# Optimization experiments

Hardware: AMD Instinct MI355X
Metric: run time of the kernel (lower is better)

The kernel has to match this reference:

```python
import jax, jax.numpy as jnp
import numpy as np

B, NS, NN = 1024, 1, 64
F = 128            # feat_dim = edge_dim = time_dim = pos_dim
DM = 4 * F         # model_dim = 512
H, DK = 2, 256     # n_head, d_k = d_v = model_dim // n_head
LN_EPS = 1e-5


def setup_inputs() -> dict:
    key = jax.random.key(0)
    ks = jax.random.split(key, 20)
    s = 0.02
    inp = {
        'src':   jax.random.normal(ks[0], (B, NS, F), jnp.float32),
        'src_t': jax.random.normal(ks[1], (B, NS, F), jnp.float32),
        'src_p': jax.random.normal(ks[2], (B, NS, F), jnp.float32),
        'seq':   jax.random.normal(ks[3], (B, NN, F), jnp.float32),
        'seq_t': jax.random.normal(ks[4], (B, NN, F), jnp.float32),
        'seq_e': jax.random.normal(ks[5], (B, NN, F), jnp.float32),
        'seq_p': jax.random.normal(ks[6], (B, NN, F), jnp.float32),
        'mask':  jax.random.randint(ks[7], (B, NS, NN), 0, 2).astype(bool),
        # MapBasedMultiHeadAttention params
        'wq': jax.random.normal(ks[8], (H * DK, DM), jnp.float32) * s,
        'wk': jax.random.normal(ks[9], (H * DK, DM), jnp.float32) * s,
        'wv': jax.random.normal(ks[10], (H * DK, DM), jnp.float32) * s,
        'wm': jax.random.normal(ks[11], (2 * DK,), jnp.float32) * s,   # weight_map: Linear(2*d_k, 1, bias=False)
        'fc_w': jax.random.normal(ks[12], (DM, H * DK), jnp.float32) * s,
        'fc_b': jnp.zeros((DM,), jnp.float32),
        'ln_g': jnp.ones((DM,), jnp.float32),
        'ln_b': jnp.zeros((DM,), jnp.float32),
        # MergeLayer(model_dim, feat_dim, feat_dim, feat_dim)
        'm1_w': jax.random.normal(ks[13], (F, DM + F), jnp.float32) * s,
        'm1_b': jnp.zeros((F,), jnp.float32),
        'm2_w': jax.random.normal(ks[14], (F, F), jnp.float32) * s,
        'm2_b': jnp.zeros((F,), jnp.float32),
    }
    return inp


def reference(src, src_t, src_p, seq, seq_t, seq_e, seq_p, mask,
              wq, wk, wv, wm, fc_w, fc_b, ln_g, ln_b, m1_w, m1_b, m2_w, m2_b):
    b, ns, f = src.shape
    nn = seq.shape[1]
    src_e = jnp.zeros((b, ns, f), src.dtype)  # edge feats of sources are zero
    q = jnp.concatenate([src, src_e, src_t, src_p], axis=-1)   # [B,NS,DM]
    k = jnp.concatenate([seq, seq_e, seq_t, seq_p], axis=-1)   # [B,NN,DM]

    # per-head projections: weight [H*DK, DM] -> [H, DK, DM]
    qh = jnp.einsum('bsd,hed->bshe', q, wq.reshape(H, DK, DM))  # [B,NS,H,DK]
    kh = jnp.einsum('bnd,hed->bnhe', k, wk.reshape(H, DK, DM))  # [B,NN,H,DK]
    vh = jnp.einsum('bnd,hed->bnhe', k, wv.reshape(H, DK, DM))  # [B,NN,H,DK]

    # weight_map(Linear over concat([q,k])) == q @ wm[:DK] + k @ wm[DK:]
    score_q = jnp.einsum('bshe,e->bhs', qh, wm[:DK])            # [B,H,NS]
    score_k = jnp.einsum('bnhe,e->bhn', kh, wm[DK:])            # [B,H,NN]
    attn = score_q[..., None] + score_k[:, :, None, :]          # [B,H,NS,NN]
    attn = jnp.where(mask[:, None, :, :], jnp.float32(-1e10), attn)
    attn = jax.nn.softmax(attn, axis=-1)

    out = jnp.einsum('bhsn,bnhe->bshe', attn, vh).reshape(b, ns, H * DK)
    out = jnp.einsum('bsd,ed->bse', out, fc_w) + fc_b           # fc
    out = jnp.where(out >= 0, out, 0.2 * out)                   # LeakyReLU(0.2)
    out = out + q                                               # residual
    mu = out.mean(axis=-1, keepdims=True)
    var = out.var(axis=-1, keepdims=True)
    out = (out - mu) / jnp.sqrt(var + LN_EPS) * ln_g + ln_b     # LayerNorm

    # MergeLayer (non_linear=True)
    x = jnp.concatenate([out, src], axis=-1)                    # [B,NS,DM+F]
    hdn = jax.nn.relu(jnp.einsum('bsd,ed->bse', x, m1_w) + m1_b)
    z = jnp.einsum('bsd,ed->bse', hdn, m2_w) + m2_b             # [B,NS,F]

    # attn in original layout: [n_head*B, len_q, len_k]
    attn_flat = attn.transpose(1, 0, 2, 3).reshape(H * b, ns, nn)
    return (z, attn_flat)
```

## Files before the change

kernel.cpp:

```cpp
#include <hip/hip_runtime.h>
#include <hip/hip_bf16.h>
#include <stdint.h>

#define B_   1024
#define NN_  64
#define F_   128
#define DM_  512
#define DK_  256

typedef unsigned short u16;
using f32x4  = __attribute__((ext_vector_type(4))) float;
using bf16x8 = __attribute__((ext_vector_type(8))) short;

__device__ __forceinline__ uint32_t f2bf(float x) {
  uint32_t u = __builtin_bit_cast(uint32_t, x);
  return (u + 0x7fffu + ((u >> 16) & 1u)) >> 16;
}
__device__ __forceinline__ float bf2f(uint32_t us) {
  return __builtin_bit_cast(float, us << 16);
}
__device__ __forceinline__ void split_pack(float x, float y, uint32_t& hp, uint32_t& lp) {
  uint32_t hx = f2bf(x), hy = f2bf(y);
  uint32_t lx = f2bf(x - bf2f(hx)), ly = f2bf(y - bf2f(hy));
  hp = hx | (hy << 16);
  lp = lx | (ly << 16);
}
__device__ __forceinline__ void split1(float x, u16& h, u16& l) {
  uint32_t hx = f2bf(x);
  h = (u16)hx;
  l = (u16)f2bf(x - bf2f(hx));
}

__global__ __launch_bounds__(256) void k_prep(
    const float* __restrict__ wv, const float* __restrict__ fc_w,
    const float* __restrict__ m1_w, const float* __restrict__ m2_w,
    const float* __restrict__ wk, const float* __restrict__ wm,
    u16* __restrict__ fc_hi, u16* __restrict__ fc_lo,
    u16* __restrict__ wvT_hi, u16* __restrict__ wvT_lo,
    u16* __restrict__ m1_hi, u16* __restrict__ m1_lo,
    u16* __restrict__ m2_hi, u16* __restrict__ m2_lo,
    float* __restrict__ wkc) {
  __shared__ float tile[32][33];
  int tid = threadIdx.x;
  int bx = blockIdx.x;

  if (bx >= 256) {
    int t = bx - 256;
    int h = t >> 3, dc = t & 7;
    int w = tid >> 6, l = tid & 63;
    int d = dc * 64 + l;
    const float* base = wk + (size_t)(h * DK_ + w * 64) * DM_ + d;
    float sacc[8] = {0.f, 0.f, 0.f, 0.f, 0.f, 0.f, 0.f, 0.f};
    #pragma unroll
    for (int e = 0; e < 64; ++e)
      sacc[e & 7] += base[e * DM_] * wm[DK_ + w * 64 + e];
    float s = ((sacc[0] + sacc[1]) + (sacc[2] + sacc[3])) +
              ((sacc[4] + sacc[5]) + (sacc[6] + sacc[7]));
    float* part = &tile[0][0];
    part[w * 64 + l] = s;
    __syncthreads();
    if (w == 0)
      wkc[h * DM_ + d] = part[l] + part[64 + l] + part[128 + l] + part[192 + l];
    return;
  }

  int gtid = bx * 256 + tid;
  int nthr = 256 * 256;
  for (int i = gtid; i < DM_ * DM_; i += nthr) split1(fc_w[i], fc_hi[i], fc_lo[i]);
  for (int i = gtid; i < F_ * (DM_ + F_); i += nthr) split1(m1_w[i], m1_hi[i], m1_lo[i]);
  for (int i = gtid; i < F_ * F_; i += nthr) split1(m2_w[i], m2_hi[i], m2_lo[i]);

  int e0 = (bx >> 4) * 32, d0 = (bx & 15) * 32;
  int rr = tid >> 3, c4 = (tid & 7) * 4;
  float4 v = *(const float4*)(wv + (e0 + rr) * DM_ + d0 + c4);
  tile[rr][c4] = v.x; tile[rr][c4 + 1] = v.y;
  tile[rr][c4 + 2] = v.z; tile[rr][c4 + 3] = v.w;
  __syncthreads();
  int dr = tid >> 3, ec = (tid & 7) * 4;
  #pragma unroll
  for (int q = 0; q < 4; ++q) {
    int idx = (d0 + dr) * DM_ + e0 + ec + q;
    split1(tile[ec + q][dr], wvT_hi[idx], wvT_lo[idx]);
  }
}

__device__ __forceinline__ f32x4 mfma_tile_split(
    const u16* __restrict__ Ahi, const u16* __restrict__ Alo, int lda,
    const u16* __restrict__ Bhi, const u16* __restrict__ Blo, int ldb, int K) {
  int l = threadIdx.x & 63;
  int r = l & 15, g = l >> 4;
  int offA = r * lda + g * 8;
  int offB = r * ldb + g * 8;
  f32x4 acc = {0.f, 0.f, 0.f, 0.f};
  for (int k = 0; k < K; k += 32) {
    bf16x8 ah = *(const bf16x8*)(Ahi + offA + k);
    bf16x8 al = *(const bf16x8*)(Alo + offA + k);
    bf16x8 bh = *(const bf16x8*)(Bhi + offB + k);
    bf16x8 bl = *(const bf16x8*)(Blo + offB + k);
    acc = __builtin_amdgcn_mfma_f32_16x16x32_bf16(ah, bh, acc, 0, 0, 0);
    acc = __builtin_amdgcn_mfma_f32_16x16x32_bf16(ah, bl, acc, 0, 0, 0);
    acc = __builtin_amdgcn_mfma_f32_16x16x32_bf16(al, bh, acc, 0, 0, 0);
  }
  return acc;
}

__global__ __launch_bounds__(256) void k_wcomb(
    const u16* __restrict__ fc_hi, const u16* __restrict__ fc_lo,
    const u16* __restrict__ wvT_hi, const u16* __restrict__ wvT_lo,
    u16* __restrict__ wc_hi, u16* __restrict__ wc_lo) {
  int wid = threadIdx.x >> 6;
  int n0g = blockIdx.y * 32;
  int h = n0g >> 9, d0 = n0g & 511;
  int m0 = blockIdx.x * 32 + (wid >> 1) * 16;
  int nb = d0 + (wid & 1) * 16;
  f32x4 acc = mfma_tile_split(fc_hi + m0 * DM_ + h * DK_,
                              fc_lo + m0 * DM_ + h * DK_, DM_,
                              wvT_hi + nb * DM_ + h * DK_,
                              wvT_lo + nb * DM_ + h * DK_, DM_, DK_);
  int l = threadIdx.x & 63, r = l & 15, g = l >> 4;
  #pragma unroll
  for (int i = 0; i < 4; ++i) {
    int m = m0 + g * 4 + i;
    int idx = m * 1024 + n0g + (wid & 1) * 16 + r;
    split1(acc[i], wc_hi[idx], wc_lo[idx]);
  }
}

__global__ __launch_bounds__(256) void k_attn(
    const float* __restrict__ seq, const float* __restrict__ seq_e,
    const float* __restrict__ seq_t, const float* __restrict__ seq_p,
    const int* __restrict__ mask, const float* __restrict__ wkc,
    float* __restrict__ attn_out,
    uint32_t* __restrict__ kbar_hi, uint32_t* __restrict__ kbar_lo) {
  __shared__ u16 kls[64][512];
  __shared__ u16 wkb_hi[1024], wkb_lo[1024];
  __shared__ float sb[2][64];
  __shared__ float els[2][64];
  __shared__ float Zs[2];
  __shared__ int mlds[64];
  int tid = threadIdx.x, b = blockIdx.x;
  int ww = tid >> 6, l = tid & 63;
  int r16 = l & 15, kg = l >> 4;

  #pragma unroll
  for (int j = 0; j < 4; ++j) {
    int i = tid * 4 + j;
    split1(wkc[i], wkb_hi[i], wkb_lo[i]);
  }
  if (tid < 64) mlds[tid] = mask[b * 64 + tid];
  __syncthreads();

  int row = ww * 16 + r16;
  int rsw = (row & 7);
  const size_t rb = ((size_t)b * 64 + row) * 128;

  f32x4 acc = {0.f, 0.f, 0.f, 0.f};
  #pragma unroll
  for (int kk4 = 0; kk4 < 4; ++kk4) {
    float4 va[4], vb[4];
    #pragma unroll
    for (int s = 0; s < 4; ++s) {
      int kk = kk4 * 4 + s;
      int d = kk * 32 + kg * 8;
      const float* ap = (d < 128 ? seq : (d < 256 ? seq_e : (d < 384 ? seq_t : seq_p)))
                        + rb + (d & 127);
      va[s] = *(const float4*)ap;
      vb[s] = *(const float4*)(ap + 4);
    }
    #pragma unroll
    for (int s = 0; s < 4; ++s) {
      int kk = kk4 * 4 + s;
      int d = kk * 32 + kg * 8;
      int chunk = d >> 3;
      bf16x8 kh;
      kh[0] = (short)f2bf(va[s].x); kh[1] = (short)f2bf(va[s].y);
      kh[2] = (short)f2bf(va[s].z); kh[3] = (short)f2bf(va[s].w);
      kh[4] = (short)f2bf(vb[s].x); kh[5] = (short)f2bf(vb[s].y);
      kh[6] = (short)f2bf(vb[s].z); kh[7] = (short)f2bf(vb[s].w);
      *(bf16x8*)(&kls[row][(chunk ^ rsw) * 8]) = kh;
      int wo = (r16 & 1) * 512 + d;
      bf16x8 wh = *(const bf16x8*)&wkb_hi[wo];
      bf16x8 wl = *(const bf16x8*)&wkb_lo[wo];
      acc = __builtin_amdgcn_mfma_f32_16x16x32_bf16(kh, wh, acc, 0, 0, 0);
      acc = __builtin_amdgcn_mfma_f32_16x16x32_bf16(kh, wl, acc, 0, 0, 0);
    }
  }
  if (r16 < 2) {
    #pragma unroll
    for (int i = 0; i < 4; ++i)
      sb[r16][ww * 16 + kg * 4 + i] = acc[i];
  }
  __syncthreads();

  if (tid < 128) {
    int h = tid >> 6, rr = tid & 63;
    float s = sb[h][rr];
    float e = mlds[rr] ? 0.f : expf(s);
    els[h][rr] = e;
    float z = e;
    #pragma unroll
    for (int off = 32; off; off >>= 1) z += __shfl_xor(z, off);
    attn_out[(h * B_ + b) * 64 + rr] = e / z;
    if (rr == 0) Zs[h] = z;
  }
  __syncthreads();

  int L = tid;
  int ch = L >> 2, bo = 2 * (L & 3);
  float a00 = 0.f, a01 = 0.f, a10 = 0.f, a11 = 0.f;
  #pragma unroll 8
  for (int j = 0; j < 64; ++j) {
    uint32_t u = *(const uint32_t*)&kls[j][((ch ^ (j & 7))) * 8 + bo];
    float f0 = bf2f(u & 0xffffu), f1 = bf2f(u >> 16);
    float e0 = els[0][j], e1 = els[1][j];
    a00 += e0 * f0; a01 += e0 * f1;
    a10 += e1 * f0; a11 += e1 * f1;
  }
  float r0 = 1.f / Zs[0], r1 = 1.f / Zs[1];
  uint32_t hp, lp;
  int idx = b * 512 + L;
  split_pack(a00 * r0, a01 * r0, hp, lp);
  kbar_hi[idx] = hp; kbar_lo[idx] = lp;
  split_pack(a10 * r1, a11 * r1, hp, lp);
  kbar_hi[idx + 256] = hp; kbar_lo[idx + 256] = lp;
}

__global__ __launch_bounds__(256) void k_fc(
    const u16* __restrict__ kb_hi, const u16* __restrict__ kb_lo,
    const u16* __restrict__ wc_hi, const u16* __restrict__ wc_lo,
    const float* __restrict__ fc_b,
    const float* __restrict__ src, const float* __restrict__ src_t,
    const float* __restrict__ src_p, float* __restrict__ fco) {
  int tid = threadIdx.x;
  int wid = tid >> 6, l = tid & 63;
  int r = l & 15, g = l >> 4;
  int m0 = blockIdx.x * 32 + (wid >> 1) * 16;
  int n0 = blockIdx.y * 64 + (wid & 1) * 32;
  int offA  = (m0 + r) * 1024 + g * 8;
  int offB0 = (n0 + r) * 1024 + g * 8;
  int offB1 = offB0 + 16 * 1024;
  f32x4 acc0 = {0.f, 0.f, 0.f, 0.f}, acc1 = {0.f, 0.f, 0.f, 0.f};
  #pragma unroll 4
  for (int k = 0; k < 1024; k += 32) {
    bf16x8 ah  = *(const bf16x8*)(kb_hi + offA + k);
    bf16x8 al  = *(const bf16x8*)(kb_lo + offA + k);
    bf16x8 b0h = *(const bf16x8*)(wc_hi + offB0 + k);
    bf16x8 b0l = *(const bf16x8*)(wc_lo + offB0 + k);
    bf16x8 b1h = *(const bf16x8*)(wc_hi + offB1 + k);
    bf16x8 b1l = *(const bf16x8*)(wc_lo + offB1 + k);
    acc0 = __builtin_amdgcn_mfma_f32_16x16x32_bf16(ah, b0h, acc0, 0, 0, 0);
    acc0 = __builtin_amdgcn_mfma_f32_16x16x32_bf16(ah, b0l, acc0, 0, 0, 0);
    acc0 = __builtin_amdgcn_mfma_f32_16x16x32_bf16(al, b0h, acc0, 0, 0, 0);
    acc1 = __builtin_amdgcn_mfma_f32_16x16x32_bf16(ah, b1h, acc1, 0, 0, 0);
    acc1 = __builtin_amdgcn_mfma_f32_16x16x32_bf16(ah, b1l, acc1, 0, 0, 0);
    acc1 = __builtin_amdgcn_mfma_f32_16x16x32_bf16(al, b1h, acc1, 0, 0, 0);
  }
  #pragma unroll
  for (int f = 0; f < 2; ++f) {
    int col = n0 + f * 16 + r;
    int part = col >> 7, fc2 = col & 127;
    float bias = fc_b[col];
    const float* qsrc = (part == 0 ? src : (part == 2 ? src_t : src_p));
    #pragma unroll
    for (int i = 0; i < 4; ++i) {
      int m = m0 + g * 4 + i;
      float c = (f == 0 ? acc0[i] : acc1[i]) + bias;
      c = (c >= 0.f) ? c : 0.2f * c;
      float qv = (part == 1) ? 0.f : qsrc[m * 128 + fc2];
      fco[m * 512 + col] = c + qv;
    }
  }
}

__global__ __launch_bounds__(512) void k_m12(
    const float* __restrict__ fco, const float* __restrict__ ln_g,
    const float* __restrict__ ln_b, const float* __restrict__ src,
    const u16* __restrict__ m1_hi, const u16* __restrict__ m1_lo,
    const float* __restrict__ m1_b,
    const u16* __restrict__ m2_hi, const u16* __restrict__ m2_lo,
    const float* __restrict__ m2_b, float* __restrict__ z) {
  __shared__ u16 xh[16][648], xl[16][648];
  __shared__ u16 hh[16][136], hl[16][136];
  int tid = threadIdx.x;
  int m0 = blockIdx.x * 16;

  {
    int row = tid >> 5, l32 = tid & 31;
    int grow = m0 + row;
    float v[16];
    float s = 0.f, s2 = 0.f;
    #pragma unroll
    for (int q = 0; q < 16; ++q) {
      v[q] = fco[grow * 512 + q * 32 + l32];
      s += v[q]; s2 += v[q] * v[q];
    }
    #pragma unroll
    for (int off = 16; off; off >>= 1) {
      s += __shfl_xor(s, off, 32);
      s2 += __shfl_xor(s2, off, 32);
    }
    float mu = s * (1.f / 512.f);
    float var = s2 * (1.f / 512.f) - mu * mu;
    float rstd = rsqrtf(var + 1e-5f);
    #pragma unroll
    for (int q = 0; q < 16; ++q) {
      int col = q * 32 + l32;
      float o = (v[q] - mu) * rstd * ln_g[col] + ln_b[col];
      split1(o, xh[row][col], xl[row][col]);
    }
    #pragma unroll
    for (int q2 = 0; q2 < 4; ++q2) {
      int c = q2 * 32 + l32;
      split1(src[grow * 128 + c], xh[row][512 + c], xl[row][512 + c]);
    }
  }
  __syncthreads();

  int wid = tid >> 6, l = tid & 63;
  int r = l & 15, g = l >> 4;
  int nb = wid * 16;
  {
    f32x4 acc = mfma_tile_split(&xh[0][0], &xl[0][0], 648,
                                m1_hi + nb * 640, m1_lo + nb * 640, 640, 640);
    int col = nb + r;
    float bias = m1_b[col];
    #pragma unroll
    for (int ii = 0; ii < 4; ++ii) {
      int row = g * 4 + ii;
      float o = fmaxf(acc[ii] + bias, 0.f);
      split1(o, hh[row][col], hl[row][col]);
    }
  }
  __syncthreads();
  {
    f32x4 acc = mfma_tile_split(&hh[0][0], &hl[0][0], 136,
                                m2_hi + nb * 128, m2_lo + nb * 128, 128, 128);
    int col = nb + r;
    float bias = m2_b[col];
    #pragma unroll
    for (int ii = 0; ii < 4; ++ii) {
      int row = g * 4 + ii;
      z[(m0 + row) * 128 + col] = acc[ii] + bias;
    }
  }
}

extern "C" void kernel_launch(void* const* d_in, const int* in_sizes, int n_in,
                              void* d_out, int out_size, void* d_ws, size_t ws_size,
                              hipStream_t stream) {
  (void)in_sizes; (void)n_in; (void)out_size; (void)ws_size;
  const float* src   = (const float*)d_in[0];
  const float* src_t = (const float*)d_in[1];
  const float* src_p = (const float*)d_in[2];
  const float* seq   = (const float*)d_in[3];
  const float* seq_t = (const float*)d_in[4];
  const float* seq_e = (const float*)d_in[5];
  const float* seq_p = (const float*)d_in[6];
  const int*   mask  = (const int*)d_in[7];
  const float* wk   = (const float*)d_in[9];
  const float* wv   = (const float*)d_in[10];
  const float* wm   = (const float*)d_in[11];
  const float* fc_w = (const float*)d_in[12];
  const float* fc_b = (const float*)d_in[13];
  const float* ln_g = (const float*)d_in[14];
  const float* ln_b = (const float*)d_in[15];
  const float* m1_w = (const float*)d_in[16];
  const float* m1_b = (const float*)d_in[17];
  const float* m2_w = (const float*)d_in[18];
  const float* m2_b = (const float*)d_in[19];

  float* z_out    = (float*)d_out;
  float* attn_out = z_out + B_ * F_;

  char* ws = (char*)d_ws;
  float* wkc     = (float*)(ws + 0);
  u16* fc_hi     = (u16*)(ws + 4096);
  u16* fc_lo     = (u16*)(ws + 528384);
  u16* m1_hi     = (u16*)(ws + 1052672);
  u16* m1_lo     = (u16*)(ws + 1216512);
  u16* m2_hi     = (u16*)(ws + 1380352);
  u16* m2_lo     = (u16*)(ws + 1413120);
  u16* wvT_hi    = (u16*)(ws + 1445888);
  u16* wvT_lo    = (u16*)(ws + 1970176);
  u16* wc_hi     = (u16*)(ws + 2494464);
  u16* wc_lo     = (u16*)(ws + 3543040);
  uint32_t* kbhi = (uint32_t*)(ws + 4591616);
  uint32_t* kblo = (uint32_t*)(ws + 6688768);
  float* fco     = (float*)(ws + 8785920);

  hipLaunchKernelGGL(k_prep, dim3(272), dim3(256), 0, stream,
                     wv, fc_w, m1_w, m2_w, wk, wm,
                     fc_hi, fc_lo, wvT_hi, wvT_lo,
                     m1_hi, m1_lo, m2_hi, m2_lo, wkc);
  hipLaunchKernelGGL(k_attn, dim3(1024), dim3(256), 0, stream,
                     seq, seq_e, seq_t, seq_p, mask, wkc,
                     attn_out, kbhi, kblo);
  hipLaunchKernelGGL(k_wcomb, dim3(16, 32), dim3(256), 0, stream,
                     fc_hi, fc_lo, wvT_hi, wvT_lo, wc_hi, wc_lo);
  hipLaunchKernelGGL(k_fc, dim3(32, 8), dim3(256), 0, stream,
                     (const u16*)kbhi, (const u16*)kblo, wc_hi, wc_lo, fc_b,
                     src, src_t, src_p, fco);
  hipLaunchKernelGGL(k_m12, dim3(64), dim3(512), 0, stream,
                     fco, ln_g, ln_b, src,
                     m1_hi, m1_lo, m1_b, m2_hi, m2_lo, m2_b, z_out);
}
```

Before: 82.62 us.

## Drop LDS key tile in k_attn; re-read fp32 keys from global for weighted sum

Removes the 64KB bf16 shared-memory copy of the key rows. The attention-weighted key sum now re-reads fp32 keys from global memory (mostly L2 hits), prefetching the next chunk under a software double buffer. Plain __syncthreads is replaced by an LDS-only waitcnt plus s_barrier so outstanding global loads are not drained at the barriers. This lowers LDS use per block, which should allow more resident blocks, and keeps full fp32 precision in the weighted sum. The cost is extra global/L2 traffic and more registers held by the prefetch buffers.

```diff
diff --git a/kernel.cpp b/kernel.cpp
--- a/kernel.cpp
+++ b/kernel.cpp
@@ -29,6 +29,10 @@
   uint32_t hx = f2bf(x);
   h = (u16)hx;
   l = (u16)f2bf(x - bf2f(hx));
+}
+__device__ __forceinline__ void bar_lgkm() {
+  asm volatile("s_waitcnt lgkmcnt(0)" ::: "memory");
+  __builtin_amdgcn_s_barrier();
 }
 
 __global__ __launch_bounds__(256) void k_prep(
@@ -132,7 +136,6 @@
     const int* __restrict__ mask, const float* __restrict__ wkc,
     float* __restrict__ attn_out,
     uint32_t* __restrict__ kbar_hi, uint32_t* __restrict__ kbar_lo) {
-  __shared__ u16 kls[64][512];
   __shared__ u16 wkb_hi[1024], wkb_lo[1024];
   __shared__ float sb[2][64];
   __shared__ float els[2][64];
@@ -150,8 +153,8 @@
   if (tid < 64) mlds[tid] = mask[b * 64 + tid];
   __syncthreads();
 
+  const float* arr = (ww == 0 ? seq : (ww == 1 ? seq_e : (ww == 2 ? seq_t : seq_p)));
   int row = ww * 16 + r16;
-  int rsw = (row & 7);
   const size_t rb = ((size_t)b * 64 + row) * 128;
 
   f32x4 acc = {0.f, 0.f, 0.f, 0.f};
@@ -160,8 +163,7 @@
     float4 va[4], vb[4];
     #pragma unroll
     for (int s = 0; s < 4; ++s) {
-      int kk = kk4 * 4 + s;
-      int d = kk * 32 + kg * 8;
+      int d = (kk4 * 4 + s) * 32 + kg * 8;
       const float* ap = (d < 128 ? seq : (d < 256 ? seq_e : (d < 384 ? seq_t : seq_p)))
                         + rb + (d & 127);
       va[s] = *(const float4*)ap;
@@ -169,15 +171,12 @@
     }
     #pragma unroll
     for (int s = 0; s < 4; ++s) {
-      int kk = kk4 * 4 + s;
-      int d = kk * 32 + kg * 8;
-      int chunk = d >> 3;
+      int d = (kk4 * 4 + s) * 32 + kg * 8;
       bf16x8 kh;
       kh[0] = (short)f2bf(va[s].x); kh[1] = (short)f2bf(va[s].y);
       kh[2] = (short)f2bf(va[s].z); kh[3] = (short)f2bf(va[s].w);
       kh[4] = (short)f2bf(vb[s].x); kh[5] = (short)f2bf(vb[s].y);
       kh[6] = (short)f2bf(vb[s].z); kh[7] = (short)f2bf(vb[s].w);
-      *(bf16x8*)(&kls[row][(chunk ^ rsw) * 8]) = kh;
       int wo = (r16 & 1) * 512 + d;
       bf16x8 wh = *(const bf16x8*)&wkb_hi[wo];
       bf16x8 wl = *(const bf16x8*)&wkb_lo[wo];
@@ -190,7 +189,14 @@
     for (int i = 0; i < 4; ++i)
       sb[r16][ww * 16 + kg * 4 + i] = acc[i];
   }
-  __syncthreads();
+
+  const float* colp = arr + (size_t)b * 8192 + 2 * l;
+  float2 v[8];
+  #pragma unroll
+  for (int u = 0; u < 8; ++u)
+    v[u] = *(const float2*)(colp + (size_t)u * 128);
+
+  bar_lgkm();
 
   if (tid < 128) {
     int h = tid >> 6, rr = tid & 63;
@@ -203,22 +209,31 @@
     attn_out[(h * B_ + b) * 64 + rr] = e / z;
     if (rr == 0) Zs[h] = z;
   }
-  __syncthreads();
-
-  int L = tid;
-  int ch = L >> 2, bo = 2 * (L & 3);
+  bar_lgkm();
+
   float a00 = 0.f, a01 = 0.f, a10 = 0.f, a11 = 0.f;
-  #pragma unroll 8
-  for (int j = 0; j < 64; ++j) {
-    uint32_t u = *(const uint32_t*)&kls[j][((ch ^ (j & 7))) * 8 + bo];
-    float f0 = bf2f(u & 0xffffu), f1 = bf2f(u >> 16);
-    float e0 = els[0][j], e1 = els[1][j];
-    a00 += e0 * f0; a01 += e0 * f1;
-    a10 += e1 * f0; a11 += e1 * f1;
+  for (int jb = 0; jb < 64; jb += 8) {
+    float2 vn[8];
+    if (jb < 56) {
+      #pragma unroll
+      for (int u = 0; u < 8; ++u)
+        vn[u] = *(const float2*)(colp + (size_t)(jb + 8 + u) * 128);
+    }
+    #pragma unroll
+    for (int u = 0; u < 8; ++u) {
+      int j = jb + u;
+      float e0 = els[0][j], e1 = els[1][j];
+      a00 += e0 * v[u].x; a01 += e0 * v[u].y;
+      a10 += e1 * v[u].x; a11 += e1 * v[u].y;
+    }
+    if (jb < 56) {
+      #pragma unroll
+      for (int u = 0; u < 8; ++u) v[u] = vn[u];
+    }
   }
   float r0 = 1.f / Zs[0], r1 = 1.f / Zs[1];
   uint32_t hp, lp;
-  int idx = b * 512 + L;
+  int idx = b * 512 + tid;
   split_pack(a00 * r0, a01 * r0, hp, lp);
   kbar_hi[idx] = hp; kbar_lo[idx] = lp;
   split_pack(a10 * r1, a11 * r1, hp, lp);
```

Result: slower. 94.69 us (+14.6%).
